# Kernel tuning notes

Measured on AMD Instinct MI355X. Metric: run time of the kernel, lower is better.

Reference implementation:

```python
import jax, jax.numpy as jnp
import numpy as np

HEAD = 8

def setup_inputs() -> dict:
    key = jax.random.key(0)
    k1, k2 = jax.random.split(key)
    B, S, D = 4, 2048, 512
    x = jax.random.normal(k1, (B, S, D), dtype=jnp.float32)
    Wq = jax.random.normal(k2, (D, D), dtype=jnp.float32) * (1.0 / np.sqrt(D))
    return {"x": x, "Wq": Wq}


def reference(x, Wq):
    # Faithful to source: Q, K, V all use linear_q (bug preserved).
    B, S, D = x.shape
    hd = D // HEAD
    q = jnp.einsum('bsd,de->bse', x, Wq)
    # Q = K = V = q
    qh = q.reshape(B, S, HEAD, hd).transpose(0, 2, 1, 3)  # [B,H,S,hd]
    # scale by sqrt(head_dim): inputs.shape[-1] inside ScaleDotAttentionLayer
    scores = jnp.einsum('bhqd,bhkd->bhqk', qh, qh) / jnp.sqrt(jnp.float32(hd))
    weights = jax.nn.softmax(scores, axis=-1)
    ctx = jnp.einsum('bhqk,bhkd->bhqd', weights, qh)
    out = ctx.transpose(0, 2, 1, 3).reshape(B, S, D)
    return out
```

## Files before the change

### kernel.cpp

```cpp
#include <hip/hip_runtime.h>
#include <hip/hip_fp16.h>
#include <math.h>

#define SS 2048
#define DD 512
#define NH 8
#define HD 64

typedef __attribute__((ext_vector_type(8))) short frag_ab;
typedef __attribute__((ext_vector_type(4))) float frag_cd;

static __device__ inline unsigned int pack_h2(float x, float y) {
    __half2 t = __floats2half2_rn(x, y);
    return *(unsigned int*)&t;
}

__global__ __launch_bounds__(256, 4) void gemm_kernel(const float* __restrict__ x,
                                                      const float* __restrict__ w,
                                                      unsigned short* __restrict__ q) {
    __shared__ __align__(16) unsigned short Ah[2][64 * 72];
    __shared__ __align__(16) unsigned short Bt[2][64 * 72];
    const int tid = threadIdx.x;
    const int lane = tid & 63, wv = tid >> 6;
    const int a = lane & 15, g = lane >> 4;
    const int bm = blockIdx.x, bn = blockIdx.y;

    frag_cd acc[4] = {};
    const int asr = tid >> 4;
    const int ac4 = (tid & 15) * 4;
    const int bnn = (tid & 31) * 2;
    const int bkk = (tid >> 5) * 8;

    float4 av[4];
    float2 bv[8];
    #pragma unroll
    for (int p = 0; p < 4; ++p)
        av[p] = *(const float4*)(x + (size_t)(bm * 64 + asr + p * 16) * 512 + ac4);
    #pragma unroll
    for (int j = 0; j < 8; ++j)
        bv[j] = *(const float2*)(w + (size_t)(bkk + j) * 512 + bn * 64 + bnn);

    for (int it = 0; it < 8; ++it) {
        const int cur = it & 1;
        #pragma unroll
        for (int p = 0; p < 4; ++p) {
            uint2 hh = { pack_h2(av[p].x, av[p].y), pack_h2(av[p].z, av[p].w) };
            *(uint2*)&Ah[cur][(asr + p * 16) * 72 + ac4] = hh;
        }
        {
            unsigned int t0[4], t1[4];
            #pragma unroll
            for (int j = 0; j < 4; ++j) {
                t0[j] = pack_h2(bv[2 * j].x, bv[2 * j + 1].x);
                t1[j] = pack_h2(bv[2 * j].y, bv[2 * j + 1].y);
            }
            *(uint4*)&Bt[cur][bnn * 72 + bkk]       = *(uint4*)t0;
            *(uint4*)&Bt[cur][(bnn + 1) * 72 + bkk] = *(uint4*)t1;
        }
        __syncthreads();
        if (it < 7) {
            const int k0 = (it + 1) * 64;
            #pragma unroll
            for (int p = 0; p < 4; ++p)
                av[p] = *(const float4*)(x + (size_t)(bm * 64 + asr + p * 16) * 512 + k0 + ac4);
            #pragma unroll
            for (int j = 0; j < 8; ++j)
                bv[j] = *(const float2*)(w + (size_t)(k0 + bkk + j) * 512 + bn * 64 + bnn);
        }
        #pragma unroll
        for (int kh = 0; kh < 2; ++kh) {
            const frag_ab bf = *(const frag_ab*)&Bt[cur][(wv * 16 + a) * 72 + kh * 32 + g * 8];
            #pragma unroll
            for (int mt = 0; mt < 4; ++mt) {
                const frag_ab af = *(const frag_ab*)&Ah[cur][(mt * 16 + a) * 72 + kh * 32 + g * 8];
                acc[mt] = __builtin_amdgcn_mfma_f32_16x16x32_f16(af, bf, acc[mt], 0, 0, 0);
            }
        }
    }
    #pragma unroll
    for (int mt = 0; mt < 4; ++mt)
        #pragma unroll
        for (int r = 0; r < 4; ++r) {
            const int m = bm * 64 + mt * 16 + g * 4 + r;
            const int n = bn * 64 + wv * 16 + a;
            __half hv = __float2half_rn(acc[mt][r]);
            q[(size_t)m * 512 + n] = *(unsigned short*)&hv;
        }
}

__global__ __launch_bounds__(512, 4) void attn_kernel(const __half* __restrict__ qg,
                                                      float* __restrict__ out) {
    __shared__ __align__(16) unsigned short Kt[2][64 * 72];
    __shared__ __align__(16) unsigned short Vt[2][64 * 72];
    __shared__ __align__(16) unsigned short Pq[8][32 * 72];

    const int tid = threadIdx.x;
    const int lane = tid & 63, wv = tid >> 6;
    const int a = lane & 15, g = lane >> 4;
    const int qq = wv & 3;
    const int kv = wv >> 2;
    const int bid = blockIdx.x;
    const int qt = bid & 15;
    const int h  = (bid >> 4) & 7;
    const int b  = bid >> 7;

    const unsigned short* qbh = (const unsigned short*)qg + (size_t)b * SS * DD + h * HD;
    const int qrow0 = qt * 128 + qq * 32;

    frag_ab qf[2][2];
    const __half2 qsc = __float2half2_rn(0.18033688011112042f);
    #pragma unroll
    for (int nt = 0; nt < 2; ++nt)
        #pragma unroll
        for (int kh = 0; kh < 2; ++kh) {
            frag_ab t = *(const frag_ab*)(qbh + (size_t)(qrow0 + nt * 16 + a) * DD + kh * 32 + g * 8);
            __half2* ph = (__half2*)&t;
            #pragma unroll
            for (int i = 0; i < 4; ++i) ph[i] = __hmul2(ph[i], qsc);
            qf[nt][kh] = t;
        }

    frag_cd oacc[4][2] = {};
    float lsum[2] = {0.f, 0.f};

    const int t8 = tid & 255;
    const int f0 = (t8 & 31) * 2;
    const int r0 = (t8 >> 5) * 8;
    const int keybase = (tid >> 8) * 1024;
    unsigned short* Ks = Kt[tid >> 8];
    unsigned short* Vs = Vt[tid >> 8];
    unsigned short* myP = Pq[wv];

    unsigned int d[8];
    #pragma unroll
    for (int k = 0; k < 8; ++k)
        d[k] = *(const unsigned int*)(qbh + (size_t)(keybase + r0 + k) * DD + f0);

    for (int it = 0; it < 16; ++it) {
        __syncthreads();
        #pragma unroll
        for (int k = 0; k < 8; ++k)
            *(unsigned int*)&Ks[(r0 + k) * 72 + f0] = d[k];
        {
            unsigned int vlo[4], vhi[4];
            #pragma unroll
            for (int j = 0; j < 4; ++j) {
                vlo[j] = (d[2 * j] & 0xFFFFu) | (d[2 * j + 1] << 16);
                vhi[j] = (d[2 * j] >> 16)     | (d[2 * j + 1] & 0xFFFF0000u);
            }
            *(uint4*)&Vs[f0 * 72 + r0]       = *(uint4*)vlo;
            *(uint4*)&Vs[(f0 + 1) * 72 + r0] = *(uint4*)vhi;
        }
        __syncthreads();

        if (it + 1 < 16) {
            const int kb = keybase + (it + 1) * 64;
            #pragma unroll
            for (int k = 0; k < 8; ++k)
                d[k] = *(const unsigned int*)(qbh + (size_t)(kb + r0 + k) * DD + f0);
        }

        const unsigned short* Kc = Kt[kv];
        const unsigned short* Vc = Vt[kv];

        #pragma unroll
        for (int kt = 0; kt < 4; ++kt) {
            const frag_ab ka0 = *(const frag_ab*)&Kc[(kt * 16 + a) * 72 + g * 8];
            const frag_ab ka1 = *(const frag_ab*)&Kc[(kt * 16 + a) * 72 + 32 + g * 8];
            #pragma unroll
            for (int nt = 0; nt < 2; ++nt) {
                frag_cd c = {};
                c = __builtin_amdgcn_mfma_f32_16x16x32_f16(ka0, qf[nt][0], c, 0, 0, 0);
                c = __builtin_amdgcn_mfma_f32_16x16x32_f16(ka1, qf[nt][1], c, 0, 0, 0);
                const float p0 = __builtin_amdgcn_exp2f(c[0] - 11.541560327111707f);
                const float p1 = __builtin_amdgcn_exp2f(c[1] - 11.541560327111707f);
                const float p2 = __builtin_amdgcn_exp2f(c[2] - 11.541560327111707f);
                const float p3 = __builtin_amdgcn_exp2f(c[3] - 11.541560327111707f);
                lsum[nt] += (p0 + p1) + (p2 + p3);
                uint2 pw = { pack_h2(p0, p1), pack_h2(p2, p3) };
                *(uint2*)&myP[(nt * 16 + a) * 72 + kt * 16 + g * 4] = pw;
            }
        }
        #pragma unroll
        for (int kh = 0; kh < 2; ++kh) {
            frag_ab va[4], pb[2];
            #pragma unroll
            for (int ft = 0; ft < 4; ++ft)
                va[ft] = *(const frag_ab*)&Vc[(ft * 16 + a) * 72 + kh * 32 + g * 8];
            #pragma unroll
            for (int nt = 0; nt < 2; ++nt)
                pb[nt] = *(const frag_ab*)&myP[(nt * 16 + a) * 72 + kh * 32 + g * 8];
            #pragma unroll
            for (int ft = 0; ft < 4; ++ft)
                #pragma unroll
                for (int nt = 0; nt < 2; ++nt)
                    oacc[ft][nt] = __builtin_amdgcn_mfma_f32_16x16x32_f16(va[ft], pb[nt], oacc[ft][nt], 0, 0, 0);
        }
    }

    #pragma unroll
    for (int nt = 0; nt < 2; ++nt) {
        lsum[nt] += __shfl_xor(lsum[nt], 16, 64);
        lsum[nt] += __shfl_xor(lsum[nt], 32, 64);
    }
    __syncthreads();
    float* Obuf = (float*)&Pq[0][0];
    float* Lbuf = (float*)&Kt[0][0];
    if (kv == 1) {
        #pragma unroll
        for (int ft = 0; ft < 4; ++ft)
            #pragma unroll
            for (int nt = 0; nt < 2; ++nt)
                #pragma unroll
                for (int r = 0; r < 4; ++r)
                    Obuf[qq * 2112 + (ft * 16 + g * 4 + r) * 33 + nt * 16 + a] = oacc[ft][nt][r];
        if (g == 0)
            #pragma unroll
            for (int nt = 0; nt < 2; ++nt)
                Lbuf[qq * 32 + nt * 16 + a] = lsum[nt];
    }
    __syncthreads();
    if (kv == 0) {
        #pragma unroll
        for (int nt = 0; nt < 2; ++nt) {
            const float inv = 1.f / (lsum[nt] + Lbuf[qq * 32 + nt * 16 + a]);
            float* op = out + ((size_t)b * SS + qrow0 + nt * 16 + a) * DD + h * HD;
            #pragma unroll
            for (int ft = 0; ft < 4; ++ft) {
                const int fb = ft * 16 + g * 4;
                float4 vv = {
                    (oacc[ft][nt][0] + Obuf[qq * 2112 + (fb + 0) * 33 + nt * 16 + a]) * inv,
                    (oacc[ft][nt][1] + Obuf[qq * 2112 + (fb + 1) * 33 + nt * 16 + a]) * inv,
                    (oacc[ft][nt][2] + Obuf[qq * 2112 + (fb + 2) * 33 + nt * 16 + a]) * inv,
                    (oacc[ft][nt][3] + Obuf[qq * 2112 + (fb + 3) * 33 + nt * 16 + a]) * inv };
                *(float4*)(op + fb) = vv;
            }
        }
    }
}

extern "C" void kernel_launch(void* const* d_in, const int* in_sizes, int n_in,
                              void* d_out, int out_size, void* d_ws, size_t ws_size,
                              hipStream_t stream) {
    const float* x  = (const float*)d_in[0];
    const float* wq = (const float*)d_in[1];
    float* out = (float*)d_out;
    unsigned short* q_h = (unsigned short*)d_ws;

    dim3 ggrid(128, 8);
    gemm_kernel<<<ggrid, 256, 0, stream>>>(x, wq, q_h);
    attn_kernel<<<512, 512, 0, stream>>>((const __half*)q_h, out);
}
```

Baseline: 127.8 us.

## Swizzle K/V shared tiles and pass P through bpermute instead of LDS

```diff
diff --git a/kernel.cpp b/kernel.cpp
--- a/kernel.cpp
+++ b/kernel.cpp
@@ -88,15 +88,16 @@
         }
 }
 
-__global__ __launch_bounds__(512, 4) void attn_kernel(const __half* __restrict__ qg,
+__global__ __launch_bounds__(512, 6) void attn_kernel(const __half* __restrict__ qg,
                                                       float* __restrict__ out) {
-    __shared__ __align__(16) unsigned short Kt[2][64 * 72];
-    __shared__ __align__(16) unsigned short Vt[2][64 * 72];
-    __shared__ __align__(16) unsigned short Pq[8][32 * 72];
+    __shared__ __align__(16) char smem[34304];
+    unsigned short* Kt = (unsigned short*)smem;
+    unsigned short* Vt = (unsigned short*)smem + 8192;
 
     const int tid = threadIdx.x;
     const int lane = tid & 63, wv = tid >> 6;
     const int a = lane & 15, g = lane >> 4;
+    const int a7 = a & 7;
     const int qq = wv & 3;
     const int kv = wv >> 2;
     const int bid = blockIdx.x;
@@ -123,24 +124,34 @@
     frag_cd oacc[4][2] = {};
     float lsum[2] = {0.f, 0.f};
 
+    const int pidx0 = ((lane & 15) + ((lane & 16) << 1)) << 2;
+    const int pidx1 = pidx0 + 64;
+    const bool ghi = (lane >= 32);
+
     const int t8 = tid & 255;
     const int f0 = (t8 & 31) * 2;
-    const int r0 = (t8 >> 5) * 8;
+    const int u8 = t8 >> 5;
+    const int r0 = u8 * 8;
     const int keybase = (tid >> 8) * 1024;
-    unsigned short* Ks = Kt[tid >> 8];
-    unsigned short* Vs = Vt[tid >> 8];
-    unsigned short* myP = Pq[wv];
+    unsigned short* Ks = Kt + (tid >> 8) * 4096;
+    unsigned short* Vs = Vt + (tid >> 8) * 4096;
+    const int kc = f0 >> 3;
+    const int ki = f0 & 7;
 
     unsigned int d[8];
     #pragma unroll
     for (int k = 0; k < 8; ++k)
         d[k] = *(const unsigned int*)(qbh + (size_t)(keybase + r0 + k) * DD + f0);
 
+    const unsigned short* Kc = Kt + kv * 4096;
+    const unsigned short* Vc = Vt + kv * 4096;
+    const float coff = -11.541560327111707f;
+
     for (int it = 0; it < 16; ++it) {
         __syncthreads();
         #pragma unroll
         for (int k = 0; k < 8; ++k)
-            *(unsigned int*)&Ks[(r0 + k) * 72 + f0] = d[k];
+            *(unsigned int*)&Ks[(r0 + k) * 64 + ((kc ^ k) << 3) + ki] = d[k];
         {
             unsigned int vlo[4], vhi[4];
             #pragma unroll
@@ -148,8 +159,8 @@
                 vlo[j] = (d[2 * j] & 0xFFFFu) | (d[2 * j + 1] << 16);
                 vhi[j] = (d[2 * j] >> 16)     | (d[2 * j + 1] & 0xFFFF0000u);
             }
-            *(uint4*)&Vs[f0 * 72 + r0]       = *(uint4*)vlo;
-            *(uint4*)&Vs[(f0 + 1) * 72 + r0] = *(uint4*)vhi;
+            *(uint4*)&Vs[f0 * 64 + ((u8 ^ (f0 & 7)) << 3)]             = *(uint4*)vlo;
+            *(uint4*)&Vs[(f0 + 1) * 64 + ((u8 ^ ((f0 + 1) & 7)) << 3)] = *(uint4*)vhi;
         }
         __syncthreads();
 
@@ -160,41 +171,51 @@
                 d[k] = *(const unsigned int*)(qbh + (size_t)(kb + r0 + k) * DD + f0);
         }
 
-        const unsigned short* Kc = Kt[kv];
-        const unsigned short* Vc = Vt[kv];
-
+        unsigned int u[2][4][2];
         #pragma unroll
         for (int kt = 0; kt < 4; ++kt) {
-            const frag_ab ka0 = *(const frag_ab*)&Kc[(kt * 16 + a) * 72 + g * 8];
-            const frag_ab ka1 = *(const frag_ab*)&Kc[(kt * 16 + a) * 72 + 32 + g * 8];
+            const frag_ab ka0 = *(const frag_ab*)&Kc[(kt * 16 + a) * 64 + ((g ^ a7) << 3)];
+            const frag_ab ka1 = *(const frag_ab*)&Kc[(kt * 16 + a) * 64 + (((4 + g) ^ a7) << 3)];
             #pragma unroll
             for (int nt = 0; nt < 2; ++nt) {
-                frag_cd c = {};
+                frag_cd c = {coff, coff, coff, coff};
                 c = __builtin_amdgcn_mfma_f32_16x16x32_f16(ka0, qf[nt][0], c, 0, 0, 0);
                 c = __builtin_amdgcn_mfma_f32_16x16x32_f16(ka1, qf[nt][1], c, 0, 0, 0);
-                const float p0 = __builtin_amdgcn_exp2f(c[0] - 11.541560327111707f);
-                const float p1 = __builtin_amdgcn_exp2f(c[1] - 11.541560327111707f);
-                const float p2 = __builtin_amdgcn_exp2f(c[2] - 11.541560327111707f);
-                const float p3 = __builtin_amdgcn_exp2f(c[3] - 11.541560327111707f);
+                const float p0 = __builtin_amdgcn_exp2f(c[0]);
+                const float p1 = __builtin_amdgcn_exp2f(c[1]);
+                const float p2 = __builtin_amdgcn_exp2f(c[2]);
+                const float p3 = __builtin_amdgcn_exp2f(c[3]);
                 lsum[nt] += (p0 + p1) + (p2 + p3);
-                uint2 pw = { pack_h2(p0, p1), pack_h2(p2, p3) };
-                *(uint2*)&myP[(nt * 16 + a) * 72 + kt * 16 + g * 4] = pw;
+                u[nt][kt][0] = pack_h2(p0, p1);
+                u[nt][kt][1] = pack_h2(p2, p3);
             }
         }
         #pragma unroll
         for (int kh = 0; kh < 2; ++kh) {
-            frag_ab va[4], pb[2];
-            #pragma unroll
-            for (int ft = 0; ft < 4; ++ft)
-                va[ft] = *(const frag_ab*)&Vc[(ft * 16 + a) * 72 + kh * 32 + g * 8];
-            #pragma unroll
-            for (int nt = 0; nt < 2; ++nt)
-                pb[nt] = *(const frag_ab*)&myP[(nt * 16 + a) * 72 + kh * 32 + g * 8];
-            #pragma unroll
-            for (int ft = 0; ft < 4; ++ft)
-                #pragma unroll
-                for (int nt = 0; nt < 2; ++nt)
-                    oacc[ft][nt] = __builtin_amdgcn_mfma_f32_16x16x32_f16(va[ft], pb[nt], oacc[ft][nt], 0, 0, 0);
+            frag_ab pb[2];
+            #pragma unroll
+            for (int nt = 0; nt < 2; ++nt) {
+                const int lo0 = __builtin_amdgcn_ds_bpermute(pidx0, (int)u[nt][2 * kh][0]);
+                const int hi0 = __builtin_amdgcn_ds_bpermute(pidx0, (int)u[nt][2 * kh + 1][0]);
+                const int lo1 = __builtin_amdgcn_ds_bpermute(pidx0, (int)u[nt][2 * kh][1]);
+                const int hi1 = __builtin_amdgcn_ds_bpermute(pidx0, (int)u[nt][2 * kh + 1][1]);
+                const int lo2 = __builtin_amdgcn_ds_bpermute(pidx1, (int)u[nt][2 * kh][0]);
+                const int hi2 = __builtin_amdgcn_ds_bpermute(pidx1, (int)u[nt][2 * kh + 1][0]);
+                const int lo3 = __builtin_amdgcn_ds_bpermute(pidx1, (int)u[nt][2 * kh][1]);
+                const int hi3 = __builtin_amdgcn_ds_bpermute(pidx1, (int)u[nt][2 * kh + 1][1]);
+                union { unsigned int w[4]; frag_ab f; } pu;
+                pu.w[0] = (unsigned int)(ghi ? hi0 : lo0);
+                pu.w[1] = (unsigned int)(ghi ? hi1 : lo1);
+                pu.w[2] = (unsigned int)(ghi ? hi2 : lo2);
+                pu.w[3] = (unsigned int)(ghi ? hi3 : lo3);
+                pb[nt] = pu.f;
+            }
+            #pragma unroll
+            for (int ft = 0; ft < 4; ++ft) {
+                const frag_ab va = *(const frag_ab*)&Vc[(ft * 16 + a) * 64 + (((4 * kh + g) ^ a7) << 3)];
+                oacc[ft][0] = __builtin_amdgcn_mfma_f32_16x16x32_f16(va, pb[0], oacc[ft][0], 0, 0, 0);
+                oacc[ft][1] = __builtin_amdgcn_mfma_f32_16x16x32_f16(va, pb[1], oacc[ft][1], 0, 0, 0);
+            }
         }
     }
 
@@ -204,8 +225,8 @@
         lsum[nt] += __shfl_xor(lsum[nt], 32, 64);
     }
     __syncthreads();
-    float* Obuf = (float*)&Pq[0][0];
-    float* Lbuf = (float*)&Kt[0][0];
+    float* Obuf = (float*)smem;
+    float* Lbuf = (float*)(smem + 33792);
     if (kv == 1) {
         #pragma unroll
         for (int ft = 0; ft < 4; ++ft)
```

Measured after the change: 306.4 us. +139.7%, slower.
